# Kernel optimization log

Hardware: AMD Instinct MI355X
Metric: run time of the kernel (lower is better)

The kernel has to match this reference:

```python
import jax, jax.numpy as jnp
import numpy as np

B, IN, OUT, FAN = 2048, 4096, 4096, 64

def setup_inputs() -> dict:
    key = jax.random.key(0)
    k1, k2, k3, k4 = jax.random.split(key, 4)
    input = jax.random.normal(k1, (B, IN), dtype=jnp.float32)
    condensed_weight = jax.random.normal(k2, (OUT, FAN), dtype=jnp.float32) * 0.05
    bias = jax.random.normal(k3, (OUT,), dtype=jnp.float32) * 0.05
    input_mask = jax.random.randint(k4, (OUT, FAN), 0, IN, dtype=jnp.int64)
    return {"input": input, "condensed_weight": condensed_weight,
            "bias": bias, "input_mask": input_mask}

def reference(input, condensed_weight, bias, input_mask):
    # Per output neuron o: sum_f input[b, idx[o,f]] * w[o,f] + bias[o]
    # gathered: [B, OUT, FAN] -- the structured-sparse gather
    gathered = jnp.take(input, input_mask, axis=1)
    return jnp.einsum("bof,of->bo", gathered, condensed_weight) + bias
```

## Files before the change

### kernel.cpp

```cpp
#include <hip/hip_runtime.h>

#define B_DIM   2048
#define IN_DIM  4096
#define OUT_DIM 4096
#define FAN     64


typedef float v2f __attribute__((ext_vector_type(2)));

__device__ __forceinline__ unsigned bf16_rne(float f) {
    unsigned u = __float_as_uint(f);
    return (u + 0x7fffu + ((u >> 16) & 1u)) >> 16;
}

__global__ __launch_bounds__(256) void pack_kernel(
    const float* __restrict__ input, uint4* __restrict__ wsp)
{
    const int idx = blockIdx.x * 256 + threadIdx.x;
    const int t   = idx >> 11;
    const int c0  = (idx & 2047) << 1;

    const float* p = input + (size_t)t * 8 * IN_DIM + c0;
    float2 r[8];
    #pragma unroll
    for (int i = 0; i < 8; ++i)
        r[i] = *reinterpret_cast<const float2*>(p + i * IN_DIM);

    uint4 q0, q1;
    q0.x = bf16_rne(r[0].x) | (bf16_rne(r[1].x) << 16);
    q0.y = bf16_rne(r[2].x) | (bf16_rne(r[3].x) << 16);
    q0.z = bf16_rne(r[4].x) | (bf16_rne(r[5].x) << 16);
    q0.w = bf16_rne(r[6].x) | (bf16_rne(r[7].x) << 16);
    q1.x = bf16_rne(r[0].y) | (bf16_rne(r[1].y) << 16);
    q1.y = bf16_rne(r[2].y) | (bf16_rne(r[3].y) << 16);
    q1.z = bf16_rne(r[4].y) | (bf16_rne(r[5].y) << 16);
    q1.w = bf16_rne(r[6].y) | (bf16_rne(r[7].y) << 16);

    wsp[(size_t)t * 4096 + c0 + 0] = q0;
    wsp[(size_t)t * 4096 + c0 + 1] = q1;
}

__global__ __launch_bounds__(512, 1) void condensed_kernel(
    const uint4* __restrict__ wsp,
    const float* __restrict__ weight,
    const float* __restrict__ bias,
    const int*   __restrict__ mask,
    float*       __restrict__ out)
{
    __shared__ __align__(16) uint4 lds[8192];

    const int tid     = threadIdx.x;
    const int o       = blockIdx.y * 512 + tid;
    const int tbase   = blockIdx.x * 8;
    const int rowbase = blockIdx.x * 64;

    unsigned addrs[FAN];
    float    wv[FAN];
    {
        const int4*   mv = reinterpret_cast<const int4*>(mask)     + o * (FAN / 4);
        const float4* wp = reinterpret_cast<const float4*>(weight) + o * (FAN / 4);
        #pragma unroll
        for (int j = 0; j < FAN / 4; ++j) {
            int4   m4 = mv[j];
            float4 w4 = wp[j];
            addrs[4*j+0] = (unsigned)m4.x << 4;
            addrs[4*j+1] = (unsigned)m4.y << 4;
            addrs[4*j+2] = (unsigned)m4.z << 4;
            addrs[4*j+3] = (unsigned)m4.w << 4;
            wv[4*j+0] = w4.x;
            wv[4*j+1] = w4.y;
            wv[4*j+2] = w4.z;
            wv[4*j+3] = w4.w;
        }
    }
    const float bv = bias[o];

    {
        const uint4* src = wsp + (size_t)tbase * 4096 + tid;
        #pragma unroll
        for (int it = 0; it < 8; ++it) {
            __builtin_amdgcn_global_load_lds(
                (const __attribute__((address_space(1))) unsigned*)(src + it * 512),
                (__attribute__((address_space(3))) unsigned*)(lds + it * 512 + tid),
                16, 0, 0);
        }
    }
    __syncthreads();

    const char* ldsb = reinterpret_cast<const char*>(lds);

    for (int hp = 0; hp < 4; ++hp) {
        {
            const uint4* src = wsp + (size_t)(tbase + 2 * hp + 1) * 4096 + tid;
            #pragma unroll
            for (int it = 0; it < 8; ++it) {
                __builtin_amdgcn_global_load_lds(
                    (const __attribute__((address_space(1))) unsigned*)(src + it * 512),
                    (__attribute__((address_space(3))) unsigned*)(lds + 4096 + it * 512 + tid),
                    16, 0, 0);
            }
        }
        {
            v2f a01 = {0.f, 0.f}, a23 = {0.f, 0.f}, a45 = {0.f, 0.f}, a67 = {0.f, 0.f};
            #pragma unroll
            for (int j = 0; j < FAN; ++j) {
                const uint4 g = *reinterpret_cast<const uint4*>(ldsb + addrs[j]);
                const v2f w2 = {wv[j], wv[j]};
                v2f v;
                v.x = __uint_as_float(g.x << 16);
                v.y = __uint_as_float(g.x & 0xffff0000u);
                a01 = __builtin_elementwise_fma(v, w2, a01);
                v.x = __uint_as_float(g.y << 16);
                v.y = __uint_as_float(g.y & 0xffff0000u);
                a23 = __builtin_elementwise_fma(v, w2, a23);
                v.x = __uint_as_float(g.z << 16);
                v.y = __uint_as_float(g.z & 0xffff0000u);
                a45 = __builtin_elementwise_fma(v, w2, a45);
                v.x = __uint_as_float(g.w << 16);
                v.y = __uint_as_float(g.w & 0xffff0000u);
                a67 = __builtin_elementwise_fma(v, w2, a67);
            }
            float* op = out + (size_t)(rowbase + 8 * (2 * hp)) * OUT_DIM + o;
            op[0 * OUT_DIM] = a01.x + bv;
            op[1 * OUT_DIM] = a01.y + bv;
            op[2 * OUT_DIM] = a23.x + bv;
            op[3 * OUT_DIM] = a23.y + bv;
            op[4 * OUT_DIM] = a45.x + bv;
            op[5 * OUT_DIM] = a45.y + bv;
            op[6 * OUT_DIM] = a67.x + bv;
            op[7 * OUT_DIM] = a67.y + bv;
        }
        __syncthreads();

        if (hp < 3) {
            const uint4* src = wsp + (size_t)(tbase + 2 * hp + 2) * 4096 + tid;
            #pragma unroll
            for (int it = 0; it < 8; ++it) {
                __builtin_amdgcn_global_load_lds(
                    (const __attribute__((address_space(1))) unsigned*)(src + it * 512),
                    (__attribute__((address_space(3))) unsigned*)(lds + it * 512 + tid),
                    16, 0, 0);
            }
        }
        {
            v2f a01 = {0.f, 0.f}, a23 = {0.f, 0.f}, a45 = {0.f, 0.f}, a67 = {0.f, 0.f};
            #pragma unroll
            for (int j = 0; j < FAN; ++j) {
                const uint4 g = *reinterpret_cast<const uint4*>(ldsb + 65536 + addrs[j]);
                const v2f w2 = {wv[j], wv[j]};
                v2f v;
                v.x = __uint_as_float(g.x << 16);
                v.y = __uint_as_float(g.x & 0xffff0000u);
                a01 = __builtin_elementwise_fma(v, w2, a01);
                v.x = __uint_as_float(g.y << 16);
                v.y = __uint_as_float(g.y & 0xffff0000u);
                a23 = __builtin_elementwise_fma(v, w2, a23);
                v.x = __uint_as_float(g.z << 16);
                v.y = __uint_as_float(g.z & 0xffff0000u);
                a45 = __builtin_elementwise_fma(v, w2, a45);
                v.x = __uint_as_float(g.w << 16);
                v.y = __uint_as_float(g.w & 0xffff0000u);
                a67 = __builtin_elementwise_fma(v, w2, a67);
            }
            float* op = out + (size_t)(rowbase + 8 * (2 * hp + 1)) * OUT_DIM + o;
            op[0 * OUT_DIM] = a01.x + bv;
            op[1 * OUT_DIM] = a01.y + bv;
            op[2 * OUT_DIM] = a23.x + bv;
            op[3 * OUT_DIM] = a23.y + bv;
            op[4 * OUT_DIM] = a45.x + bv;
            op[5 * OUT_DIM] = a45.y + bv;
            op[6 * OUT_DIM] = a67.x + bv;
            op[7 * OUT_DIM] = a67.y + bv;
        }
        __syncthreads();
    }
}

extern "C" void kernel_launch(void* const* d_in, const int* in_sizes, int n_in,
                              void* d_out, int out_size, void* d_ws, size_t ws_size,
                              hipStream_t stream) {
    const float* input  = (const float*)d_in[0];
    const float* weight = (const float*)d_in[1];
    const float* bias   = (const float*)d_in[2];
    const int*   mask   = (const int*)d_in[3];
    float*       out    = (float*)d_out;
    uint4*       wsp    = (uint4*)d_ws;

    pack_kernel<<<2048, 256, 0, stream>>>(input, wsp);
    dim3 grid(32, 8);
    condensed_kernel<<<grid, 512, 0, stream>>>(wsp, weight, bias, mask, out);
}
```

Measured before the change: 133.4 us.

## Split each output's fan-in across two lanes with DPP reduction

Each output neuron is now handled by a pair of lanes, each holding half of the 64 mask indices and weights, which halves per-thread register arrays. Partial sums are combined with a DPP xor-1 swizzle and only the even lane writes. The grid is reshaped so each block covers 256 outputs and 128 batch rows, which doubles the number of LDS tile stages per block. The aim is to cut register pressure and the serial dependency chain per thread. The costs are a shuffle per output, half the lanes idle during stores, and LDS tiles loaded twice as often relative to outputs.

```diff
diff --git a/kernel.cpp b/kernel.cpp
--- a/kernel.cpp
+++ b/kernel.cpp
@@ -11,6 +11,11 @@
 __device__ __forceinline__ unsigned bf16_rne(float f) {
     unsigned u = __float_as_uint(f);
     return (u + 0x7fffu + ((u >> 16) & 1u)) >> 16;
+}
+
+__device__ __forceinline__ float xor1_sum(float x) {
+    int p = __builtin_amdgcn_update_dpp(0, __float_as_int(x), 0xB1, 0xF, 0xF, true);
+    return x + __int_as_float(p);
 }
 
 __global__ __launch_bounds__(256) void pack_kernel(
@@ -50,17 +55,19 @@
     __shared__ __align__(16) uint4 lds[8192];
 
     const int tid     = threadIdx.x;
-    const int o       = blockIdx.y * 512 + tid;
-    const int tbase   = blockIdx.x * 8;
-    const int rowbase = blockIdx.x * 64;
-
-    unsigned addrs[FAN];
-    float    wv[FAN];
+    const int h       = tid & 1;
+    const int ol      = tid >> 1;
+    const int o       = blockIdx.y * 256 + ol;
+    const int tbase   = blockIdx.x * 16;
+    const int rowbase = blockIdx.x * 128;
+
+    unsigned addrs[FAN / 2];
+    float    wv[FAN / 2];
     {
-        const int4*   mv = reinterpret_cast<const int4*>(mask)     + o * (FAN / 4);
-        const float4* wp = reinterpret_cast<const float4*>(weight) + o * (FAN / 4);
+        const int4*   mv = reinterpret_cast<const int4*>(mask   + o * FAN + h * 32);
+        const float4* wp = reinterpret_cast<const float4*>(weight + o * FAN + h * 32);
         #pragma unroll
-        for (int j = 0; j < FAN / 4; ++j) {
+        for (int j = 0; j < 8; ++j) {
             int4   m4 = mv[j];
             float4 w4 = wp[j];
             addrs[4*j+0] = (unsigned)m4.x << 4;
@@ -73,6 +80,11 @@
             wv[4*j+3] = w4.w;
         }
     }
+    #pragma unroll
+    for (int j = 0; j < FAN / 2; ++j) {
+        asm volatile("" : "+v"(addrs[j]));
+        asm volatile("" : "+v"(wv[j]));
+    }
     const float bv = bias[o];
 
     {
@@ -89,7 +101,7 @@
 
     const char* ldsb = reinterpret_cast<const char*>(lds);
 
-    for (int hp = 0; hp < 4; ++hp) {
+    for (int hp = 0; hp < 8; ++hp) {
         {
             const uint4* src = wsp + (size_t)(tbase + 2 * hp + 1) * 4096 + tid;
             #pragma unroll
@@ -103,7 +115,7 @@
         {
             v2f a01 = {0.f, 0.f}, a23 = {0.f, 0.f}, a45 = {0.f, 0.f}, a67 = {0.f, 0.f};
             #pragma unroll
-            for (int j = 0; j < FAN; ++j) {
+            for (int j = 0; j < FAN / 2; ++j) {
                 const uint4 g = *reinterpret_cast<const uint4*>(ldsb + addrs[j]);
                 const v2f w2 = {wv[j], wv[j]};
                 v2f v;
@@ -120,19 +132,25 @@
                 v.y = __uint_as_float(g.w & 0xffff0000u);
                 a67 = __builtin_elementwise_fma(v, w2, a67);
             }
-            float* op = out + (size_t)(rowbase + 8 * (2 * hp)) * OUT_DIM + o;
-            op[0 * OUT_DIM] = a01.x + bv;
-            op[1 * OUT_DIM] = a01.y + bv;
-            op[2 * OUT_DIM] = a23.x + bv;
-            op[3 * OUT_DIM] = a23.y + bv;
-            op[4 * OUT_DIM] = a45.x + bv;
-            op[5 * OUT_DIM] = a45.y + bv;
-            op[6 * OUT_DIM] = a67.x + bv;
-            op[7 * OUT_DIM] = a67.y + bv;
+            const float s0 = xor1_sum(a01.x), s1 = xor1_sum(a01.y);
+            const float s2 = xor1_sum(a23.x), s3 = xor1_sum(a23.y);
+            const float s4 = xor1_sum(a45.x), s5 = xor1_sum(a45.y);
+            const float s6 = xor1_sum(a67.x), s7 = xor1_sum(a67.y);
+            if (h == 0) {
+                float* op = out + (size_t)(rowbase + 8 * (2 * hp)) * OUT_DIM + o;
+                op[0 * OUT_DIM] = s0 + bv;
+                op[1 * OUT_DIM] = s1 + bv;
+                op[2 * OUT_DIM] = s2 + bv;
+                op[3 * OUT_DIM] = s3 + bv;
+                op[4 * OUT_DIM] = s4 + bv;
+                op[5 * OUT_DIM] = s5 + bv;
+                op[6 * OUT_DIM] = s6 + bv;
+                op[7 * OUT_DIM] = s7 + bv;
+            }
         }
         __syncthreads();
 
-        if (hp < 3) {
+        if (hp < 7) {
             const uint4* src = wsp + (size_t)(tbase + 2 * hp + 2) * 4096 + tid;
             #pragma unroll
             for (int it = 0; it < 8; ++it) {
@@ -145,7 +163,7 @@
         {
             v2f a01 = {0.f, 0.f}, a23 = {0.f, 0.f}, a45 = {0.f, 0.f}, a67 = {0.f, 0.f};
             #pragma unroll
-            for (int j = 0; j < FAN; ++j) {
+            for (int j = 0; j < FAN / 2; ++j) {
                 const uint4 g = *reinterpret_cast<const uint4*>(ldsb + 65536 + addrs[j]);
                 const v2f w2 = {wv[j], wv[j]};
                 v2f v;
@@ -162,15 +180,21 @@
                 v.y = __uint_as_float(g.w & 0xffff0000u);
                 a67 = __builtin_elementwise_fma(v, w2, a67);
             }
-            float* op = out + (size_t)(rowbase + 8 * (2 * hp + 1)) * OUT_DIM + o;
-            op[0 * OUT_DIM] = a01.x + bv;
-            op[1 * OUT_DIM] = a01.y + bv;
-            op[2 * OUT_DIM] = a23.x + bv;
-            op[3 * OUT_DIM] = a23.y + bv;
-            op[4 * OUT_DIM] = a45.x + bv;
-            op[5 * OUT_DIM] = a45.y + bv;
-            op[6 * OUT_DIM] = a67.x + bv;
-            op[7 * OUT_DIM] = a67.y + bv;
+            const float s0 = xor1_sum(a01.x), s1 = xor1_sum(a01.y);
+            const float s2 = xor1_sum(a23.x), s3 = xor1_sum(a23.y);
+            const float s4 = xor1_sum(a45.x), s5 = xor1_sum(a45.y);
+            const float s6 = xor1_sum(a67.x), s7 = xor1_sum(a67.y);
+            if (h == 0) {
+                float* op = out + (size_t)(rowbase + 8 * (2 * hp + 1)) * OUT_DIM + o;
+                op[0 * OUT_DIM] = s0 + bv;
+                op[1 * OUT_DIM] = s1 + bv;
+                op[2 * OUT_DIM] = s2 + bv;
+                op[3 * OUT_DIM] = s3 + bv;
+                op[4 * OUT_DIM] = s4 + bv;
+                op[5 * OUT_DIM] = s5 + bv;
+                op[6 * OUT_DIM] = s6 + bv;
+                op[7 * OUT_DIM] = s7 + bv;
+            }
         }
         __syncthreads();
     }
@@ -187,6 +211,6 @@
     uint4*       wsp    = (uint4*)d_ws;
 
     pack_kernel<<<2048, 256, 0, stream>>>(input, wsp);
-    dim3 grid(32, 8);
+    dim3 grid(16, 16);
     condensed_kernel<<<grid, 512, 0, stream>>>(wsp, weight, bias, mask, out);
 }
```

New measurement: 136.0 us. About the same (+1.9%).

## Reorder mask and weight per output to spread LDS gather bank accesses

Applied to the files above, without the earlier changes.

Adds a small pre-pass kernel that bucket-sorts each output neuron's 64 mask indices (and the matching weights) by the low three index bits. It then rotates each neuron's order by a per-lane offset (o & 7), so neighbouring lanes in a wavefront tend to read different LDS bank groups at the same loop step. The aim is to cut LDS bank conflicts in the random-gather inner loop. The cost is an extra launch, a serial per-thread pass whose writes are scattered, a changed floating-point summation order, and a dependence on the workspace being large enough.

```diff
diff --git a/kernel.cpp b/kernel.cpp
--- a/kernel.cpp
+++ b/kernel.cpp
@@ -11,6 +11,34 @@
 __device__ __forceinline__ unsigned bf16_rne(float f) {
     unsigned u = __float_as_uint(f);
     return (u + 0x7fffu + ((u >> 16) & 1u)) >> 16;
+}
+
+__global__ __launch_bounds__(256) void reorder_kernel(
+    const int* __restrict__ mask, const float* __restrict__ weight,
+    int* __restrict__ mask2, float* __restrict__ weight2)
+{
+    const int o   = blockIdx.x * 256 + threadIdx.x;
+    const unsigned rot = 8u * (unsigned)(o & 7);
+    const int*   m = mask   + o * FAN;
+    const float* w = weight + o * FAN;
+
+    unsigned long long cnt = 0ull;
+    #pragma unroll
+    for (int j = 0; j < FAN; ++j)
+        cnt += 1ull << (8 * (m[j] & 7));
+
+    unsigned long long off = cnt * 0x0101010101010100ull;
+
+    #pragma unroll
+    for (int j = 0; j < FAN; ++j) {
+        const int idx = m[j];
+        const int g   = idx & 7;
+        const unsigned p = (unsigned)(off >> (8 * g)) & 255u;
+        off += 1ull << (8 * g);
+        const int dst = (int)((p + 64u - rot) & 63u);
+        mask2[o * FAN + dst]   = idx;
+        weight2[o * FAN + dst] = w[j];
+    }
 }
 
 __global__ __launch_bounds__(256) void pack_kernel(
@@ -186,7 +214,21 @@
     float*       out    = (float*)d_out;
     uint4*       wsp    = (uint4*)d_ws;
 
+    const size_t pack_bytes = (size_t)16 * 1024 * 1024;
+    const size_t m2_bytes   = (size_t)OUT_DIM * FAN * sizeof(int);
+    const size_t w2_bytes   = (size_t)OUT_DIM * FAN * sizeof(float);
+
+    const int* use_m = mask;
+    const float* use_w = weight;
+    if (ws_size >= pack_bytes + m2_bytes + w2_bytes) {
+        int*   mask2   = (int*)((char*)d_ws + pack_bytes);
+        float* weight2 = (float*)((char*)d_ws + pack_bytes + m2_bytes);
+        reorder_kernel<<<16, 256, 0, stream>>>(mask, weight, mask2, weight2);
+        use_m = mask2;
+        use_w = weight2;
+    }
+
     pack_kernel<<<2048, 256, 0, stream>>>(input, wsp);
     dim3 grid(32, 8);
-    condensed_kernel<<<grid, 512, 0, stream>>>(wsp, weight, bias, mask, out);
-}
+    condensed_kernel<<<grid, 512, 0, stream>>>(wsp, use_w, bias, use_m, out);
+}
```

Result: slower. 161.0 us (+20.7%).
